# Performance work log

Measured on AMD Instinct MI355X. Metric: run time of the kernel, lower is better.

The kernel has to match this reference:

```python
import jax, jax.numpy as jnp
import numpy as np

EPS = 1e-6  # flax LayerNorm default
ROPE_BASE = 10000.0

def _ln(x, scale, bias):
    m = jnp.mean(x, axis=-1, keepdims=True)
    v = jnp.mean(jnp.square(x - m), axis=-1, keepdims=True)
    return (x - m) * jax.lax.rsqrt(v + EPS) * scale + bias

def _rope_cache(u, v, head_dim):
    # P = head_dim//2//2 pairs per axis
    P = head_dim // 4
    freqs = jnp.arange(P, dtype=jnp.float32) / (P - 1 + 1e-9)
    inv = 1.0 / ROPE_BASE ** freqs
    ang_x = jnp.einsum('nl,f->nlf', u, inv)
    ang_y = jnp.einsum('nl,f->nlf', v, inv)
    return jnp.cos(ang_x), jnp.sin(ang_x), jnp.cos(ang_y), jnp.sin(ang_y)

def _rope_apply(q, cos_x, sin_x, cos_y, sin_y):
    n, L, H, D = q.shape
    q = q.reshape(n, L, H, D // 2, 2)
    P = D // 4
    qx, qy = q[..., :P, :], q[..., P:, :]
    def rot(qp, c, s):
        c = c[:, :, None, :]
        s = s[:, :, None, :]
        x, y = qp[..., 0], qp[..., 1]
        return jnp.stack([x * c - y * s, x * s + y * c], axis=-1)
    return jnp.concatenate([rot(qx, cos_x, sin_x), rot(qy, cos_y, sin_y)], axis=-2).reshape(n, L, H, D)

def setup_inputs():
    key = jax.random.key(0)
    ks = jax.random.split(key, 12)
    N, HW, CIN = 8, 384, 3
    P, W, DPT, H, HD, MLP = 16, 768, 4, 12, 64, 3072
    s = 0.02
    return {
        'image': jax.random.normal(ks[0], (N, HW, HW, CIN), jnp.float32),
        'conv_kernel': jax.random.normal(ks[1], (P, P, CIN, W), jnp.float32) * s,
        'conv_bias': jnp.zeros((W,), jnp.float32),
        'ln1_scale': jnp.ones((DPT, W), jnp.float32),
        'ln1_bias': jnp.zeros((DPT, W), jnp.float32),
        'wq': jax.random.normal(ks[2], (DPT, W, H, HD), jnp.float32) * s,
        'bq': jnp.zeros((DPT, H, HD), jnp.float32),
        'wk': jax.random.normal(ks[3], (DPT, W, H, HD), jnp.float32) * s,
        'bk': jnp.zeros((DPT, H, HD), jnp.float32),
        'wv': jax.random.normal(ks[4], (DPT, W, H, HD), jnp.float32) * s,
        'bv': jnp.zeros((DPT, H, HD), jnp.float32),
        'wo': jax.random.normal(ks[5], (DPT, H, HD, W), jnp.float32) * s,
        'bo': jnp.zeros((DPT, W), jnp.float32),
        'ln2_scale': jnp.ones((DPT, W), jnp.float32),
        'ln2_bias': jnp.zeros((DPT, W), jnp.float32),
        'w1': jax.random.normal(ks[6], (DPT, W, MLP), jnp.float32) * s,
        'b1': jnp.zeros((DPT, MLP), jnp.float32),
        'w2': jax.random.normal(ks[7], (DPT, MLP, W), jnp.float32) * s,
        'b2': jnp.zeros((DPT, W), jnp.float32),
        'lnf_scale': jnp.ones((W,), jnp.float32),
        'lnf_bias': jnp.zeros((W,), jnp.float32),
    }

def reference(image, conv_kernel, conv_bias, ln1_scale, ln1_bias,
              wq, bq, wk, bk, wv, bv, wo, bo,
              ln2_scale, ln2_bias, w1, b1, w2, b2, lnf_scale, lnf_bias):
    patch = conv_kernel.shape[0]
    # patch-embedding conv, stride=patch, VALID padding (NHWC/HWIO)
    x = jax.lax.conv_general_dilated(
        image, conv_kernel, window_strides=(patch, patch), padding='VALID',
        dimension_numbers=('NHWC', 'HWIO', 'NHWC')) + conv_bias
    n, h, w, c = x.shape
    L = h * w
    x = x.reshape(n, L, c)

    depth, _, H, HD = wq.shape
    # RoPE 2D coordinates for square grid (default path when rope_uv is None)
    ys, xs = jnp.mgrid[:h, :w]
    u = jnp.tile(((xs.reshape(-1) + 0.5) / w)[None, :], [n, 1])
    v = jnp.tile(((ys.reshape(-1) + 0.5) / h)[None, :], [n, 1])
    cos_x, sin_x, cos_y, sin_y = _rope_cache(u, v, HD)

    scale = 1.0 / jnp.sqrt(jnp.float32(HD))
    for l in range(depth):
        y = _ln(x, ln1_scale[l], ln1_bias[l])
        q = jnp.einsum('nld,dhk->nlhk', y, wq[l]) + bq[l]
        k = jnp.einsum('nld,dhk->nlhk', y, wk[l]) + bk[l]
        vv = jnp.einsum('nld,dhk->nlhk', y, wv[l]) + bv[l]
        q = _rope_apply(q, cos_x, sin_x, cos_y, sin_y)
        k = _rope_apply(k, cos_x, sin_x, cos_y, sin_y)
        logits = jnp.einsum('nqhd,nkhd->nhqk', q, k) * scale
        attn = jax.nn.softmax(logits, axis=-1)
        o = jnp.einsum('nhqk,nkhd->nqhd', attn, vv)
        y = jnp.einsum('nqhd,hdo->nqo', o, wo[l]) + bo[l]
        x = x + y
        y = _ln(x, ln2_scale[l], ln2_bias[l])
        y = jax.nn.gelu(jnp.einsum('nld,df->nlf', y, w1[l]) + b1[l])
        y = jnp.einsum('nlf,fd->nld', y, w2[l]) + b2[l]
        x = x + y

    x = _ln(x, lnf_scale, lnf_bias)  # encoder_norm
    return jnp.mean(x, axis=1)       # gap pooling -> [n, width]
```

## Files before the change

### kernel.cpp

```cpp
#include <hip/hip_runtime.h>
#include <hip/hip_bf16.h>

typedef __hip_bfloat16 bf16;
typedef __bf16 bf16x8 __attribute__((ext_vector_type(8)));
typedef float f32x4  __attribute__((ext_vector_type(4)));

#define NBATCH 8
#define LTOK   576
#define NT     4608
#define CW     768
#define NH     12
#define HDIM   64
#define DEPTH  4
#define MLPW   3072
#define GRIDP  24
#define IMGS   384
#define QKVW   2304

static __device__ __forceinline__ unsigned bfpair(float a, float b){
    bf16 x = __float2bfloat16(a), y = __float2bfloat16(b);
    return ((unsigned)*(unsigned short*)&y << 16) | *(unsigned short*)&x;
}
static __device__ __forceinline__ float b2f(bf16 v){ return __bfloat162float(v); }

static __device__ __forceinline__ int xcd_swizzle(int orig, int nwg){
    int q = nwg >> 3, r = nwg & 7;
    int xcd = orig & 7, j = orig >> 3;
    int base = (xcd < r) ? xcd*(q+1) : r*(q+1) + (xcd-r)*q;
    return base + j;
}

static __device__ __forceinline__ void gl_lds16(const bf16* g, bf16* l){
    __builtin_amdgcn_global_load_lds(
        (const __attribute__((address_space(1))) unsigned int*)(const void*)g,
        (__attribute__((address_space(3))) unsigned int*)(void*)l, 16, 0, 0);
}

__global__ void rope_cache_kernel(float* __restrict__ rc){
    int idx = blockIdx.x*256 + threadIdx.x;
    if (idx >= LTOK*16) return;
    int l = idx >> 4, f = idx & 15;
    int py = l / GRIDP, px = l % GRIDP;
    float u = (px + 0.5f) / (float)GRIDP;
    float v = (py + 0.5f) / (float)GRIDP;
    float fr = (float)f / (15.0f + 1e-9f);
    float inv = expf(-fr * 9.210340371976184f);
    float sx, cx, sy, cy;
    sincosf(u * inv, &sx, &cx);
    sincosf(v * inv, &sy, &cy);
    rc[idx]         = cx;
    rc[idx + 9216]  = sx;
    rc[idx + 18432] = cy;
    rc[idx + 27648] = sy;
}

__global__ void patch_gather(const float* __restrict__ img, bf16* __restrict__ p){
    int idx = blockIdx.x*256 + threadIdx.x;
    int t = idx / CW, kk = idx % CW;
    int n = t / LTOK, l = t % LTOK;
    int py = l / GRIDP, px = l % GRIDP;
    int i = kk / 48, r = kk % 48, j = r / 3, c = r % 3;
    p[idx] = __float2bfloat16(img[((size_t)(n*IMGS + py*16 + i)*IMGS + px*16 + j)*3 + c]);
}

__global__ __launch_bounds__(256) void wtrans_b(const float* __restrict__ in, bf16* __restrict__ out,
                                                int K, int N, size_t inStride, size_t outStride){
    in  += blockIdx.z * inStride;
    out += blockIdx.z * outStride;
    __shared__ float t[32][33];
    const int n0 = blockIdx.x*32, k0 = blockIdx.y*32;
    const int tx = threadIdx.x & 31, ty = threadIdx.x >> 5;
    #pragma unroll
    for (int r = 0; r < 4; ++r)
        t[ty + 8*r][tx] = in[(size_t)(k0 + ty + 8*r)*N + n0 + tx];
    __syncthreads();
    #pragma unroll
    for (int r = 0; r < 4; ++r)
        out[(size_t)(n0 + ty + 8*r)*K + k0 + tx] = __float2bfloat16(t[tx][ty + 8*r]);
}

__global__ void bias_pack(const float* __restrict__ bq, const float* __restrict__ bk,
                          const float* __restrict__ bv, float* __restrict__ o){
    int idx = blockIdx.x*256 + threadIdx.x;
    int l = idx / QKVW, r = idx % QKVW;
    const float* src = (r < 768) ? (bq + l*768 + r) :
                       (r < 1536) ? (bk + l*768 + r - 768) : (bv + l*768 + r - 1536);
    o[idx] = *src;
}

static __device__ __forceinline__ float gelu_tanh(float x){
    float x3 = x*x*x;
    return 0.5f*x*(1.0f + tanhf(0.7978845608028654f*(x + 0.044715f*x3)));
}

template<int EPI, typename TC>
__global__ __launch_bounds__(256) void gemm_a(const bf16* __restrict__ A, int lda,
                                              const bf16* __restrict__ B, int ldb,
                                              const float* __restrict__ bias,
                                              TC* __restrict__ C, int ldc, int K,
                                              const float* __restrict__ rc){
    __shared__ bf16 As[2][128*64];
    __shared__ bf16 Bs[2][64*64];
    const int tid = threadIdx.x;
    const int w = tid >> 6, l = tid & 63;
    const int quad = l >> 4, lr = l & 15;
    const int wm = w & 1, wn = w >> 1;

    const int nwg = gridDim.x * gridDim.y;
    const int swz = xcd_swizzle(blockIdx.y * gridDim.x + blockIdx.x, nwg);
    const int rowT = (swz / gridDim.x) * 128;
    const int colT = (swz % gridDim.x) * 64;

    const int srow = l >> 3;
    const int schk = (l & 7) ^ (srow & 7);

    const bf16* Ap[4];
    const bf16* Bp[2];
    #pragma unroll
    for (int t = 0; t < 4; ++t)
        Ap[t] = A + (size_t)(rowT + (w*4+t)*8 + srow)*lda + schk*8;
    #pragma unroll
    for (int t = 0; t < 2; ++t)
        Bp[t] = B + (size_t)(colT + (w*2+t)*8 + srow)*ldb + schk*8;

    auto STAGE = [&](int k0, int buf){
        #pragma unroll
        for (int t = 0; t < 4; ++t) gl_lds16(Ap[t] + k0, &As[buf][(w*4+t)*512]);
        #pragma unroll
        for (int t = 0; t < 2; ++t) gl_lds16(Bp[t] + k0, &Bs[buf][(w*2+t)*512]);
    };

    f32x4 acc[4][2];
    #pragma unroll
    for (int i = 0; i < 4; ++i)
        #pragma unroll
        for (int j = 0; j < 2; ++j) acc[i][j] = (f32x4){0.f,0.f,0.f,0.f};

    auto KCOMP = [&](const bf16* __restrict__ Ac, const bf16* __restrict__ Bc){
        #pragma unroll
        for (int kh = 0; kh < 2; ++kh){
            bf16x8 af[4], bfr[2];
            #pragma unroll
            for (int i = 0; i < 4; ++i){
                int r = wm*64 + i*16 + lr;
                af[i] = *(const bf16x8*)(Ac + r*64 + (((kh*4 + quad) ^ (r & 7))*8));
            }
            #pragma unroll
            for (int j = 0; j < 2; ++j){
                int r = wn*32 + j*16 + lr;
                bfr[j] = *(const bf16x8*)(Bc + r*64 + (((kh*4 + quad) ^ (r & 7))*8));
            }
            #pragma unroll
            for (int i = 0; i < 4; ++i)
                #pragma unroll
                for (int j = 0; j < 2; ++j)
                    acc[i][j] = __builtin_amdgcn_mfma_f32_16x16x32_bf16(af[i], bfr[j], acc[i][j], 0, 0, 0);
        }
    };

    const int S = K >> 6;
    STAGE(0, 0);
    STAGE(64, 1);

    for (int s = 0; s < S; s += 2){
        asm volatile("s_waitcnt vmcnt(6)" ::: "memory");
        __builtin_amdgcn_s_barrier();
        asm volatile("" ::: "memory");
        KCOMP(&As[0][0], &Bs[0][0]);
        __builtin_amdgcn_s_barrier();
        if (s + 2 < S) STAGE((s + 2)*64, 0);
        if (s + 2 < S) asm volatile("s_waitcnt vmcnt(6)" ::: "memory");
        else           asm volatile("s_waitcnt vmcnt(0)" ::: "memory");
        __builtin_amdgcn_s_barrier();
        asm volatile("" ::: "memory");
        KCOMP(&As[1][0], &Bs[1][0]);
        __builtin_amdgcn_s_barrier();
        if (s + 3 < S) STAGE((s + 3)*64, 1);
    }

    #pragma unroll
    for (int i = 0; i < 4; ++i){
        #pragma unroll
        for (int j = 0; j < 2; ++j){
            const int row = rowT + wm*64 + i*16 + quad*4;
            const int col = colT + wn*32 + j*16 + lr;
            const float bb = bias ? bias[col] : 0.f;
            if (EPI == 5){
                const int hcol = col & 63;
                const int p = hcol >> 1;
                const bool isv = (col >= 1536);
                const bool isY = (p >= 16);
                const int f = p & 15;
                const int cOff = isY ? 18432 : 0;
                const int sOff = isY ? 27648 : 9216;
                #pragma unroll
                for (int r = 0; r < 4; ++r){
                    float val = acc[i][j][r] + bb;
                    float other = __shfl_xor(val, 1);
                    float outv = val;
                    if (!isv){
                        const int tok = (row + r) % LTOK;
                        const float cc = rc[cOff + tok*16 + f];
                        const float ss = rc[sOff + tok*16 + f];
                        outv = ((col & 1) == 0) ? val*cc - other*ss
                                                : other*ss + val*cc;
                    }
                    *(bf16*)(C + (size_t)(row + r)*ldc + col) = __float2bfloat16(outv);
                }
            } else {
                #pragma unroll
                for (int r = 0; r < 4; ++r){
                    float val = acc[i][j][r] + bb;
                    TC* cp = C + (size_t)(row + r)*ldc + col;
                    if (EPI == 2) val = gelu_tanh(val);
                    if (EPI == 1) val += *(float*)cp;
                    if (EPI == 0 || EPI == 2) *(bf16*)cp = __float2bfloat16(val);
                    else                      *(float*)cp = val;
                }
            }
        }
    }
}

__global__ __launch_bounds__(256) void ln_wave(const float* __restrict__ x,
                                               const float* __restrict__ sc,
                                               const float* __restrict__ bs,
                                               bf16* __restrict__ y){
    const int tid = threadIdx.x, w = tid >> 6, l = tid & 63;
    const int t = blockIdx.x*4 + w;
    const float4* xr = (const float4*)(x + (size_t)t*CW);
    float4 a[3];
    #pragma unroll
    for (int i = 0; i < 3; ++i) a[i] = xr[l + 64*i];
    float s = 0.f;
    #pragma unroll
    for (int i = 0; i < 3; ++i) s += a[i].x + a[i].y + a[i].z + a[i].w;
    #pragma unroll
    for (int off = 1; off < 64; off <<= 1) s += __shfl_xor(s, off);
    const float m = s * (1.0f/768.0f);
    float vs = 0.f;
    #pragma unroll
    for (int i = 0; i < 3; ++i){
        float dx = a[i].x-m, dy = a[i].y-m, dz = a[i].z-m, dw = a[i].w-m;
        vs += dx*dx + dy*dy + dz*dz + dw*dw;
    }
    #pragma unroll
    for (int off = 1; off < 64; off <<= 1) vs += __shfl_xor(vs, off);
    const float rs = rsqrtf(vs*(1.0f/768.0f) + 1e-6f);
    const float4* scp = (const float4*)sc;
    const float4* bsp = (const float4*)bs;
    uint2* yr = (uint2*)(y + (size_t)t*CW);
    #pragma unroll
    for (int i = 0; i < 3; ++i){
        float4 sv = scp[l + 64*i], bv = bsp[l + 64*i];
        float r0 = (a[i].x-m)*rs*sv.x + bv.x;
        float r1 = (a[i].y-m)*rs*sv.y + bv.y;
        float r2 = (a[i].z-m)*rs*sv.z + bv.z;
        float r3 = (a[i].w-m)*rs*sv.w + bv.w;
        yr[l + 64*i] = make_uint2(bfpair(r0,r1), bfpair(r2,r3));
    }
}

__global__ __launch_bounds__(256) void attn_flash(const bf16* __restrict__ qkv,
                                                  bf16* __restrict__ o){
    __shared__ bf16 Ks[64*72];
    __shared__ bf16 Vs[64*72];
    __shared__ bf16 Ps[64*72];
    __shared__ float alph[64];
    __shared__ float lsum[64];
    const int tid = threadIdx.x;
    const int w = tid >> 6, l = tid & 63;
    const int quad = l >> 4, lr = l & 15;

    const int nwg = gridDim.x * gridDim.y * gridDim.z;
    const int orig = (blockIdx.z * gridDim.y + blockIdx.y) * gridDim.x + blockIdx.x;
    const int swz = xcd_swizzle(orig, nwg);
    const int q0 = (swz % gridDim.x) * 64;
    const int t2 = swz / gridDim.x;
    const int hI = t2 % gridDim.y;
    const int nI = t2 / gridDim.y;

    const size_t tokBase = (size_t)nI * LTOK;
    const int off = hI * 64;

    bf16x8 qf[2];
    #pragma unroll
    for (int kh = 0; kh < 2; ++kh)
        qf[kh] = *(const bf16x8*)(qkv + (tokBase + q0 + w*16 + lr)*QKVW + off + kh*32 + quad*8);

    f32x4 oacc[4];
    #pragma unroll
    for (int j = 0; j < 4; ++j) oacc[j] = (f32x4){0.f,0.f,0.f,0.f};
    float m_run = -3.0e38f, l_run = 0.f;

    for (int ch = 0; ch < 9; ++ch){
        __syncthreads();
        #pragma unroll
        for (int i = 0; i < 2; ++i){
            int g = i*256 + tid, r = g >> 3, c = g & 7;
            *(uint4*)(Ks + r*72 + c*8) =
                *(const uint4*)(qkv + (tokBase + ch*64 + r)*QKVW + 768 + off + c*8);
        }
        #pragma unroll
        for (int i = 0; i < 2; ++i){
            int g = i*256 + tid, r = g >> 3, c = g & 7;
            uint4 tmp4 = *(const uint4*)(qkv + (tokBase + ch*64 + r)*QKVW + 1536 + off + c*8);
            const bf16* t8 = (const bf16*)&tmp4;
            #pragma unroll
            for (int jj = 0; jj < 8; ++jj) Vs[(c*8 + jj)*72 + r] = t8[jj];
        }
        __syncthreads();

        f32x4 st[4];
        #pragma unroll
        for (int t = 0; t < 4; ++t){
            st[t] = (f32x4){0.f,0.f,0.f,0.f};
            #pragma unroll
            for (int kh = 0; kh < 2; ++kh){
                bf16x8 kf = *(const bf16x8*)(Ks + (t*16 + lr)*72 + kh*32 + quad*8);
                st[t] = __builtin_amdgcn_mfma_f32_16x16x32_bf16(kf, qf[kh], st[t], 0, 0, 0);
            }
        }
        float lm = -3.0e38f;
        #pragma unroll
        for (int t = 0; t < 4; ++t)
            #pragma unroll
            for (int r = 0; r < 4; ++r){
                st[t][r] *= 0.125f;
                lm = fmaxf(lm, st[t][r]);
            }
        lm = fmaxf(lm, __shfl_xor(lm, 16));
        lm = fmaxf(lm, __shfl_xor(lm, 32));
        float mn = fmaxf(m_run, lm);
        float alpha = __expf(m_run - mn);
        m_run = mn;
        float ls = 0.f;
        #pragma unroll
        for (int t = 0; t < 4; ++t)
            #pragma unroll
            for (int r = 0; r < 4; ++r){
                float p = __expf(st[t][r] - mn);
                st[t][r] = p; ls += p;
            }
        ls += __shfl_xor(ls, 16);
        ls += __shfl_xor(ls, 32);
        l_run = l_run*alpha + ls;
        if ((tid & 48) == 0) alph[w*16 + lr] = alpha;
        #pragma unroll
        for (int t = 0; t < 4; ++t)
            #pragma unroll
            for (int r = 0; r < 4; ++r)
                Ps[(w*16 + lr)*72 + t*16 + quad*4 + r] = __float2bfloat16(st[t][r]);
        float af[4];
        #pragma unroll
        for (int r = 0; r < 4; ++r) af[r] = alph[w*16 + quad*4 + r];
        #pragma unroll
        for (int j = 0; j < 4; ++j)
            #pragma unroll
            for (int r = 0; r < 4; ++r) oacc[j][r] *= af[r];
        #pragma unroll
        for (int kh = 0; kh < 2; ++kh){
            bf16x8 pf = *(const bf16x8*)(Ps + (w*16 + lr)*72 + kh*32 + quad*8);
            #pragma unroll
            for (int j = 0; j < 4; ++j){
                bf16x8 vf = *(const bf16x8*)(Vs + (j*16 + lr)*72 + kh*32 + quad*8);
                oacc[j] = __builtin_amdgcn_mfma_f32_16x16x32_bf16(pf, vf, oacc[j], 0, 0, 0);
            }
        }
    }

    if ((tid & 48) == 0) lsum[w*16 + lr] = l_run;
    float linv[4];
    #pragma unroll
    for (int r = 0; r < 4; ++r) linv[r] = 1.0f / lsum[w*16 + quad*4 + r];
    #pragma unroll
    for (int j = 0; j < 4; ++j)
        #pragma unroll
        for (int r = 0; r < 4; ++r)
            o[(tokBase + q0 + w*16 + quad*4 + r)*CW + off + j*16 + lr] =
                __float2bfloat16(oacc[j][r] * linv[r]);
}

__global__ void mean_kernel(const bf16* __restrict__ y, float* __restrict__ out){
    int c = blockIdx.x*256 + threadIdx.x;
    int n = blockIdx.y;
    float s = 0.f;
    for (int l = 0; l < LTOK; ++l) s += b2f(y[((size_t)n*LTOK + l)*CW + c]);
    out[n*CW + c] = s * (1.0f/576.0f);
}

extern "C" void kernel_launch(void* const* d_in, const int* in_sizes, int n_in,
                              void* d_out, int out_size, void* d_ws, size_t ws_size,
                              hipStream_t stream){
    const float* image = (const float*)d_in[0];
    const float* convk = (const float*)d_in[1];
    const float* convb = (const float*)d_in[2];
    const float* ln1s  = (const float*)d_in[3];
    const float* ln1b  = (const float*)d_in[4];
    const float* wq    = (const float*)d_in[5];
    const float* bq    = (const float*)d_in[6];
    const float* wk    = (const float*)d_in[7];
    const float* bk    = (const float*)d_in[8];
    const float* wv    = (const float*)d_in[9];
    const float* bv    = (const float*)d_in[10];
    const float* wo    = (const float*)d_in[11];
    const float* bo    = (const float*)d_in[12];
    const float* ln2s  = (const float*)d_in[13];
    const float* ln2b  = (const float*)d_in[14];
    const float* w1    = (const float*)d_in[15];
    const float* b1    = (const float*)d_in[16];
    const float* w2    = (const float*)d_in[17];
    const float* b2    = (const float*)d_in[18];
    const float* lnfs  = (const float*)d_in[19];
    const float* lnfb  = (const float*)d_in[20];
    float* out = (float*)d_out;

    const size_t u = (size_t)NT*CW;
    float* ws    = (float*)d_ws;
    float* ropeC = ws;
    float* bqkvA = ws + 36864;
    float* x     = bqkvA + 4*QKVW;
    bf16*  y     = (bf16*)(x + u);
    bf16*  qkv   = y + u;
    bf16*  o     = qkv + (size_t)NT*QKVW;
    bf16*  h     = o + u;
    bf16*  vT    = h + (size_t)NT*MLPW;
    bf16*  convT = vT + u;
    bf16*  wqkvT = convT + 589824;
    bf16*  woT   = wqkvT + (size_t)4*QKVW*CW;
    bf16*  w1T   = woT + (size_t)4*CW*CW;
    bf16*  w2T   = w1T + (size_t)4*CW*MLPW;

    rope_cache_kernel<<<36, 256, 0, stream>>>(ropeC);
    patch_gather<<<(NT*CW)/256, 256, 0, stream>>>(image, y);
    bias_pack<<<36, 256, 0, stream>>>(bq, bk, bv, bqkvA);
    wtrans_b<<<dim3(24,24,1), 256, 0, stream>>>(convk, convT, CW, CW, 0, 0);
    wtrans_b<<<dim3(24,24,4), 256, 0, stream>>>(wq, wqkvT,           CW, CW, (size_t)CW*CW, (size_t)QKVW*CW);
    wtrans_b<<<dim3(24,24,4), 256, 0, stream>>>(wk, wqkvT + 589824,  CW, CW, (size_t)CW*CW, (size_t)QKVW*CW);
    wtrans_b<<<dim3(24,24,4), 256, 0, stream>>>(wv, wqkvT + 1179648, CW, CW, (size_t)CW*CW, (size_t)QKVW*CW);
    wtrans_b<<<dim3(24,24,4), 256, 0, stream>>>(wo, woT,             CW, CW, (size_t)CW*CW, (size_t)CW*CW);
    wtrans_b<<<dim3(96,24,4), 256, 0, stream>>>(w1, w1T,  CW, MLPW, (size_t)CW*MLPW, (size_t)CW*MLPW);
    wtrans_b<<<dim3(24,96,4), 256, 0, stream>>>(w2, w2T, MLPW,  CW, (size_t)CW*MLPW, (size_t)CW*MLPW);

    gemm_a<3,float><<<dim3(12,36), 256, 0, stream>>>(y, CW, convT, CW, convb, x, CW, CW, nullptr);

    for (int l = 0; l < DEPTH; ++l){
        ln_wave<<<NT/4, 256, 0, stream>>>(x, ln1s + l*CW, ln1b + l*CW, y);
        gemm_a<5,bf16><<<dim3(36,36), 256, 0, stream>>>(y, CW, wqkvT + (size_t)l*QKVW*CW, CW,
                                                        bqkvA + l*QKVW, qkv, QKVW, CW, ropeC);
        attn_flash<<<dim3(9, NH, NBATCH), 256, 0, stream>>>(qkv, o);
        gemm_a<1,float><<<dim3(12,36), 256, 0, stream>>>(o, CW, woT + (size_t)l*CW*CW, CW,
                                                         bo + l*CW, x, CW, CW, nullptr);
        ln_wave<<<NT/4, 256, 0, stream>>>(x, ln2s + l*CW, ln2b + l*CW, y);
        gemm_a<2,bf16><<<dim3(48,36), 256, 0, stream>>>(y, CW, w1T + (size_t)l*CW*MLPW, CW,
                                                        b1 + l*MLPW, h, MLPW, CW, nullptr);
        gemm_a<1,float><<<dim3(12,36), 256, 0, stream>>>(h, MLPW, w2T + (size_t)l*CW*MLPW, MLPW,
                                                         b2 + l*CW, x, CW, MLPW, nullptr);
    }
    ln_wave<<<NT/4, 256, 0, stream>>>(x, lnfs, lnfb, y);
    mean_kernel<<<dim3(3, NBATCH), 256, 0, stream>>>(y, out);
}
```

Measured before the change: 1.066 ms.

## Pre-transpose V in a separate kernel and simplify GEMM double-buffer loop

Adds a vtrans kernel that writes V per head in a dim-major layout, so attn_flash loads V tiles with vector stores into LDS instead of scattered scalar transposed writes repeated by every query block. The GEMM main loop is rewritten as a single-step loop with a buffer toggle instead of a manually two-way unrolled loop, and it handles odd stage counts. The change adds an extra kernel launch and an extra global round trip for V each layer.

Result: faster. 1.033 ms (-3.1%).

```diff
diff --git a/kernel.cpp b/kernel.cpp
--- a/kernel.cpp
+++ b/kernel.cpp
@@ -136,19 +136,27 @@
         #pragma unroll
         for (int j = 0; j < 2; ++j) acc[i][j] = (f32x4){0.f,0.f,0.f,0.f};
 
-    auto KCOMP = [&](const bf16* __restrict__ Ac, const bf16* __restrict__ Bc){
+    const int S = K >> 6;
+    STAGE(0, 0);
+    if (S > 1) STAGE(64, 1);
+
+    int cur = 0;
+    for (int s = 0; s < S; ++s){
+        if (s < S-1) asm volatile("s_waitcnt vmcnt(6)" ::: "memory");
+        else         asm volatile("s_waitcnt vmcnt(0)" ::: "memory");
+        __builtin_amdgcn_s_barrier();
         #pragma unroll
         for (int kh = 0; kh < 2; ++kh){
             bf16x8 af[4], bfr[2];
             #pragma unroll
             for (int i = 0; i < 4; ++i){
                 int r = wm*64 + i*16 + lr;
-                af[i] = *(const bf16x8*)(Ac + r*64 + (((kh*4 + quad) ^ (r & 7))*8));
+                af[i] = *(const bf16x8*)(&As[cur][r*64 + (((kh*4 + quad) ^ (r & 7))*8)]);
             }
             #pragma unroll
             for (int j = 0; j < 2; ++j){
                 int r = wn*32 + j*16 + lr;
-                bfr[j] = *(const bf16x8*)(Bc + r*64 + (((kh*4 + quad) ^ (r & 7))*8));
+                bfr[j] = *(const bf16x8*)(&Bs[cur][r*64 + (((kh*4 + quad) ^ (r & 7))*8)]);
             }
             #pragma unroll
             for (int i = 0; i < 4; ++i)
@@ -156,26 +164,9 @@
                 for (int j = 0; j < 2; ++j)
                     acc[i][j] = __builtin_amdgcn_mfma_f32_16x16x32_bf16(af[i], bfr[j], acc[i][j], 0, 0, 0);
         }
-    };
-
-    const int S = K >> 6;
-    STAGE(0, 0);
-    STAGE(64, 1);
-
-    for (int s = 0; s < S; s += 2){
-        asm volatile("s_waitcnt vmcnt(6)" ::: "memory");
         __builtin_amdgcn_s_barrier();
-        asm volatile("" ::: "memory");
-        KCOMP(&As[0][0], &Bs[0][0]);
-        __builtin_amdgcn_s_barrier();
-        if (s + 2 < S) STAGE((s + 2)*64, 0);
-        if (s + 2 < S) asm volatile("s_waitcnt vmcnt(6)" ::: "memory");
-        else           asm volatile("s_waitcnt vmcnt(0)" ::: "memory");
-        __builtin_amdgcn_s_barrier();
-        asm volatile("" ::: "memory");
-        KCOMP(&As[1][0], &Bs[1][0]);
-        __builtin_amdgcn_s_barrier();
-        if (s + 3 < S) STAGE((s + 3)*64, 1);
+        if (s + 2 < S) STAGE((s + 2)*64, cur);
+        cur ^= 1;
     }
 
     #pragma unroll
@@ -261,7 +252,30 @@
     }
 }
 
+__global__ __launch_bounds__(256) void vtrans(const bf16* __restrict__ qkv, bf16* __restrict__ vT){
+    __shared__ bf16 tile[64][72];
+    const int t0 = blockIdx.x*64, hI = blockIdx.y, nI = blockIdx.z;
+    const size_t base = ((size_t)nI*LTOK + t0)*QKVW + 1536 + hI*64;
+    const int tid = threadIdx.x;
+    #pragma unroll
+    for (int i = 0; i < 2; ++i){
+        int g = i*256 + tid, r = g >> 3, c = g & 7;
+        *(uint4*)&tile[r][c*8] = *(const uint4*)(qkv + base + (size_t)r*QKVW + c*8);
+    }
+    __syncthreads();
+    const size_t obase = ((size_t)(nI*NH + hI)*64)*576 + t0;
+    #pragma unroll
+    for (int i = 0; i < 2; ++i){
+        int g = i*256 + tid, d = g >> 3, c = g & 7;
+        bf16 tmp[8];
+        #pragma unroll
+        for (int j = 0; j < 8; ++j) tmp[j] = tile[c*8 + j][d];
+        *(uint4*)(vT + obase + (size_t)d*576 + c*8) = *(uint4*)tmp;
+    }
+}
+
 __global__ __launch_bounds__(256) void attn_flash(const bf16* __restrict__ qkv,
+                                                  const bf16* __restrict__ vT,
                                                   bf16* __restrict__ o){
     __shared__ bf16 Ks[64*72];
     __shared__ bf16 Vs[64*72];
@@ -282,6 +296,7 @@
 
     const size_t tokBase = (size_t)nI * LTOK;
     const int off = hI * 64;
+    const size_t vbase = ((size_t)(nI*NH + hI)*64)*576;
 
     bf16x8 qf[2];
     #pragma unroll
@@ -303,11 +318,8 @@
         }
         #pragma unroll
         for (int i = 0; i < 2; ++i){
-            int g = i*256 + tid, r = g >> 3, c = g & 7;
-            uint4 tmp4 = *(const uint4*)(qkv + (tokBase + ch*64 + r)*QKVW + 1536 + off + c*8);
-            const bf16* t8 = (const bf16*)&tmp4;
-            #pragma unroll
-            for (int jj = 0; jj < 8; ++jj) Vs[(c*8 + jj)*72 + r] = t8[jj];
+            int g = i*256 + tid, d = g >> 3, c = g & 7;
+            *(uint4*)(Vs + d*72 + c*8) = *(const uint4*)(vT + vbase + (size_t)d*576 + ch*64 + c*8);
         }
         __syncthreads();
 
@@ -448,7 +460,8 @@
         ln_wave<<<NT/4, 256, 0, stream>>>(x, ln1s + l*CW, ln1b + l*CW, y);
         gemm_a<5,bf16><<<dim3(36,36), 256, 0, stream>>>(y, CW, wqkvT + (size_t)l*QKVW*CW, CW,
                                                         bqkvA + l*QKVW, qkv, QKVW, CW, ropeC);
-        attn_flash<<<dim3(9, NH, NBATCH), 256, 0, stream>>>(qkv, o);
+        vtrans<<<dim3(9, NH, NBATCH), 256, 0, stream>>>(qkv, vT);
+        attn_flash<<<dim3(9, NH, NBATCH), 256, 0, stream>>>(qkv, vT, o);
         gemm_a<1,float><<<dim3(12,36), 256, 0, stream>>>(o, CW, woT + (size_t)l*CW*CW, CW,
                                                          bo + l*CW, x, CW, CW, nullptr);
         ln_wave<<<NT/4, 256, 0, stream>>>(x, ln2s + l*CW, ln2b + l*CW, y);
```
